# Performance work log

Measured on AMD Instinct MI355X. Metric: run time of the kernel, lower is better.

## Reference

```python
import jax, jax.numpy as jnp
import numpy as np

DIM = 1024
N_HEADS = 16
HEAD_DIM = DIM // N_HEADS
B, T = 2, 2048
ROPE_THETA = 32.0
EPS = 1e-6


def precompute_freqs_1d(dim, seq_len, theta):
    freqs = theta ** (-jnp.arange(0, dim, 2, dtype=jnp.float32) / dim)  # [dim/2]
    t = jnp.arange(seq_len, dtype=jnp.float32)
    ang = t[:, None] * freqs[None, :]  # [T, dim/2]
    return jnp.cos(ang), jnp.sin(ang)


def setup_inputs() -> dict:
    key = jax.random.key(0)
    k1, k2, k3, k4, k5 = jax.random.split(key, 5)
    x = jax.random.normal(k1, (B, T, DIM), dtype=jnp.float32)
    w_qkv = jax.random.normal(k2, (3 * DIM, DIM), dtype=jnp.float32) * (DIM ** -0.5)
    w_proj = jax.random.normal(k3, (DIM, DIM), dtype=jnp.float32) * (DIM ** -0.5)
    q_norm_w = 1.0 + 0.1 * jax.random.normal(k4, (HEAD_DIM,), dtype=jnp.float32)
    k_norm_w = 1.0 + 0.1 * jax.random.normal(k5, (HEAD_DIM,), dtype=jnp.float32)
    return {"x": x, "w_qkv": w_qkv, "w_proj": w_proj,
            "q_norm_w": q_norm_w, "k_norm_w": k_norm_w}


def _rms_norm(t, w):
    # t: [B,H,T,hd]; normalize over last dim
    var = jnp.mean(t * t, axis=-1, keepdims=True)
    return t * jax.lax.rsqrt(var + EPS) * w


def _rope(q, k, cos, sin):
    # cos/sin: [T, hd/2] -> [1,1,T,hd/2]
    cos = cos[None, None]
    sin = sin[None, None]
    q1, q2 = jnp.split(q, 2, axis=-1)
    k1, k2 = jnp.split(k, 2, axis=-1)
    q_out = jnp.concatenate([q1 * cos - q2 * sin, q2 * cos + q1 * sin], axis=-1)
    k_out = jnp.concatenate([k1 * cos - k2 * sin, k2 * cos + k1 * sin], axis=-1)
    return q_out, k_out


def reference(x, w_qkv, w_proj, q_norm_w, k_norm_w):
    Bc, Tc, C = x.shape
    scale = HEAD_DIM ** -0.5
    qkv = x @ w_qkv.T  # [B,T,3*C]
    qkv = qkv.reshape(Bc, Tc, 3, N_HEADS, HEAD_DIM).transpose(2, 0, 3, 1, 4)
    q, k, v = qkv[0], qkv[1], qkv[2]  # each [B,H,T,hd]
    q = _rms_norm(q, q_norm_w)
    k = _rms_norm(k, k_norm_w)
    cos, sin = precompute_freqs_1d(HEAD_DIM, Tc, ROPE_THETA)
    q, k = _rope(q, k, cos, sin)
    attn = jnp.einsum('bhqd,bhkd->bhqk', q, k) * scale
    causal = jnp.triu(jnp.ones((Tc, Tc), dtype=bool), k=1)
    attn = jnp.where(causal, -jnp.inf, attn)
    attn = jax.nn.softmax(attn, axis=-1)
    out = jnp.einsum('bhqk,bhkd->bhqd', attn, v)  # [B,H,T,hd]
    out = out.transpose(0, 2, 1, 3).reshape(Bc, Tc, C)
    return out @ w_proj.T
```

## Files before the change

### kernel.cpp

```cpp
#include <hip/hip_runtime.h>
#include <hip/hip_bf16.h>

#define DIM   1024
#define NH    16
#define HD    64
#define BB    2
#define TT    2048
#define BT    (BB*TT)
#define BHN   (BB*NH)

typedef __attribute__((ext_vector_type(8))) __bf16 bf16x8;
typedef __attribute__((ext_vector_type(4))) float  f32x4;

__device__ __forceinline__ unsigned short f2bf(float f) {
    unsigned int u = __float_as_uint(f);
    u = (u + 0x7fffu + ((u >> 16) & 1u)) >> 16;
    return (unsigned short)u;
}

__device__ __forceinline__ void gload_lds16(const unsigned short* g, unsigned short* l) {
    __builtin_amdgcn_global_load_lds(
        (const __attribute__((address_space(1))) unsigned int*)g,
        (__attribute__((address_space(3))) unsigned int*)l, 16, 0, 0);
}

__global__ __launch_bounds__(256) void cvt_bf16(const float* __restrict__ in,
                                                unsigned short* __restrict__ out, int n) {
    int i = blockIdx.x * 256 + threadIdx.x;
    int base = i * 8;
    if (base >= n) return;
    float4 a = *reinterpret_cast<const float4*>(in + base);
    float4 b = *reinterpret_cast<const float4*>(in + base + 4);
    uint4 o;
    o.x = (unsigned)f2bf(a.x) | ((unsigned)f2bf(a.y) << 16);
    o.y = (unsigned)f2bf(a.z) | ((unsigned)f2bf(a.w) << 16);
    o.z = (unsigned)f2bf(b.x) | ((unsigned)f2bf(b.y) << 16);
    o.w = (unsigned)f2bf(b.z) | ((unsigned)f2bf(b.w) << 16);
    *reinterpret_cast<uint4*>(out + base) = o;
}

__global__ __launch_bounds__(256) void build_rope(float* __restrict__ cosT,
                                                  float* __restrict__ sinT) {
    int i = blockIdx.x * 256 + threadIdx.x;
    if (i >= TT * 32) return;
    int t = i >> 5, j = i & 31;
    float freq = exp2f(-5.0f * (float)j * (1.0f / 32.0f));
    float ang  = (float)t * freq;
    cosT[i] = cosf(ang);
    sinT[i] = sinf(ang);
}

__global__ __launch_bounds__(256) void gemm_bt(const unsigned short* __restrict__ A,
                                               const unsigned short* __restrict__ Bt,
                                               float* __restrict__ C,
                                               int M, int N, int K) {
    __shared__ alignas(16) unsigned short sA[128 * 64];
    __shared__ alignas(16) unsigned short sB[128 * 64];
    const int t    = threadIdx.x;
    const int nb   = N >> 7;
    const int m0   = (blockIdx.x / nb) << 7;
    const int n0   = (blockIdx.x % nb) << 7;
    const int w    = t >> 6, lane = t & 63;
    const int wr   = w >> 1, wc = w & 1;
    const int lrow = lane & 15, lk = lane >> 4;
    const int r_   = t >> 3;
    const int c_   = t & 7;
    const int pg   = c_ ^ (r_ & 7);

    f32x4 acc[4][4] = {};

    for (int kt = 0; kt < K; kt += 64) {
        __syncthreads();
#pragma unroll
        for (int i = 0; i < 4; i++) {
            gload_lds16(A  + (size_t)(m0 + i * 32 + r_) * K + kt + pg * 8, sA + i * 2048 + w * 512);
            gload_lds16(Bt + (size_t)(n0 + i * 32 + r_) * K + kt + pg * 8, sB + i * 2048 + w * 512);
        }
        __syncthreads();
#pragma unroll
        for (int ks = 0; ks < 2; ks++) {
            bf16x8 af[4], bfr[4];
#pragma unroll
            for (int mi = 0; mi < 4; mi++) {
                int rowa = wr * 64 + mi * 16 + lrow;
                int ga   = (ks * 4 + lk) ^ (rowa & 7);
                af[mi]   = *reinterpret_cast<const bf16x8*>(&sA[rowa * 64 + ga * 8]);
                int rowb = wc * 64 + mi * 16 + lrow;
                int gb   = (ks * 4 + lk) ^ (rowb & 7);
                bfr[mi]  = *reinterpret_cast<const bf16x8*>(&sB[rowb * 64 + gb * 8]);
            }
#pragma unroll
            for (int mi = 0; mi < 4; mi++)
#pragma unroll
                for (int ni = 0; ni < 4; ni++)
                    acc[mi][ni] = __builtin_amdgcn_mfma_f32_16x16x32_bf16(af[mi], bfr[ni], acc[mi][ni], 0, 0, 0);
        }
    }
#pragma unroll
    for (int mi = 0; mi < 4; mi++)
#pragma unroll
        for (int ni = 0; ni < 4; ni++) {
            int row = m0 + wr * 64 + mi * 16 + lk * 4;
            int col = n0 + wc * 64 + ni * 16 + lrow;
#pragma unroll
            for (int i = 0; i < 4; i++)
                C[(size_t)(row + i) * N + col] = acc[mi][ni][i];
        }
}

__global__ __launch_bounds__(256) void norm_rope(const float* __restrict__ qkv,
                                                 const float* __restrict__ cosT,
                                                 const float* __restrict__ sinT,
                                                 const float* __restrict__ qw,
                                                 const float* __restrict__ kw,
                                                 unsigned short* __restrict__ Qo,
                                                 unsigned short* __restrict__ Ko,
                                                 unsigned short* __restrict__ Vo) {
    int wv = threadIdx.x >> 6, lane = threadIdx.x & 63;
    int rid = blockIdx.x * 4 + wv;
    int sel = rid >> 16;
    int rem = rid & 65535;
    int h   = rem & 15;
    int bt  = rem >> 4;
    int tp  = bt & (TT - 1);
    int b   = bt >> 11;
    float v = qkv[(size_t)bt * 3072 + sel * 1024 + h * 64 + lane];
    unsigned short* dst = (sel == 0) ? Qo : ((sel == 1) ? Ko : Vo);
    size_t didx = ((size_t)(b * NH + h) * TT + tp) * 64 + lane;
    float outv;
    if (sel < 2) {
        float ss = v * v;
#pragma unroll
        for (int m = 32; m; m >>= 1) ss += __shfl_xor(ss, m);
        float r = rsqrtf(ss * (1.0f / 64.0f) + 1e-6f);
        const float* wgt = sel ? kw : qw;
        float nv = v * r * wgt[lane];
        float other = __shfl_xor(nv, 32);
        int j = lane & 31;
        float c = cosT[tp * 32 + j], s = sinT[tp * 32 + j];
        outv = (lane < 32) ? (nv * c - other * s) : (nv * c + other * s);
        if (sel == 0) outv *= 0.125f * 1.4426950408889634f;
    } else {
        outv = v;
    }
    dst[didx] = f2bf(outv);
}

__global__ __launch_bounds__(256) void transpose_v(const unsigned short* __restrict__ Vb,
                                                   unsigned short* __restrict__ Vt) {
    __shared__ unsigned short s[64 * 68];
    const int t0 = blockIdx.x * 64, bh = blockIdx.y;
    const unsigned short* src = Vb + (size_t)bh * TT * 64;
    const int r = threadIdx.x >> 2, g4 = threadIdx.x & 3;
#pragma unroll
    for (int p = 0; p < 2; p++) {
        int g = g4 + p * 4;
        *reinterpret_cast<uint4*>(&s[r * 68 + g * 8]) =
            *reinterpret_cast<const uint4*>(src + (size_t)(t0 + r) * 64 + g * 8);
    }
    __syncthreads();
#pragma unroll
    for (int p = 0; p < 2; p++) {
        int tt = (g4 + p * 4) * 8;
        unsigned short tmp[8];
#pragma unroll
        for (int j = 0; j < 8; j++) tmp[j] = s[(tt + j) * 68 + r];
        *reinterpret_cast<uint4*>(Vt + ((size_t)bh * 64 + r) * TT + t0 + tt) =
            *reinterpret_cast<uint4*>(tmp);
    }
}

__global__ __launch_bounds__(256) void attn_fwd(const unsigned short* __restrict__ Qm,
                                                const unsigned short* __restrict__ Km,
                                                const unsigned short* __restrict__ Vt,
                                                unsigned short* __restrict__ Om) {
    __shared__ alignas(16) unsigned short sQ[64 * 68];
    __shared__ alignas(16) unsigned short sK[64 * 68];
    __shared__ alignas(16) unsigned short sVT[64 * 68];
    __shared__ alignas(16) unsigned short sP[4][16 * 68];
    const int bh = blockIdx.y;
    const int qt = (blockIdx.x + blockIdx.y) & 31;
    const int b = bh >> 4, h = bh & 15;
    const unsigned short* Qp = Qm + (size_t)bh * TT * 64;
    const unsigned short* Kp = Km + (size_t)bh * TT * 64;
    const unsigned short* Vp = Vt + (size_t)bh * 64 * TT;
    const int t = threadIdx.x, wv = t >> 6, lane = t & 63;
    const int lrow = lane & 15, lk = lane >> 4;
    const int r_ = t >> 3, c_ = t & 7;
    const int d_ = t >> 2, g_ = t & 3;

#pragma unroll
    for (int i = 0; i < 2; i++) {
        int r = i * 32 + r_;
        *reinterpret_cast<uint4*>(&sQ[r * 68 + c_ * 8]) =
            *reinterpret_cast<const uint4*>(Qp + (size_t)(qt * 64 + r) * 64 + c_ * 8);
    }
    uint4 kreg[2], vreg[2];
#pragma unroll
    for (int i = 0; i < 2; i++)
        kreg[i] = *reinterpret_cast<const uint4*>(Kp + (size_t)(i * 32 + r_) * 64 + c_ * 8);
#pragma unroll
    for (int p = 0; p < 2; p++)
        vreg[p] = *reinterpret_cast<const uint4*>(Vp + (size_t)d_ * TT + (g_ + p * 4) * 8);
#pragma unroll
    for (int i = 0; i < 2; i++)
        *reinterpret_cast<uint4*>(&sK[(i * 32 + r_) * 68 + c_ * 8]) = kreg[i];
#pragma unroll
    for (int p = 0; p < 2; p++)
        *reinterpret_cast<uint4*>(&sVT[d_ * 68 + (g_ + p * 4) * 8]) = vreg[p];
    __syncthreads();

    bf16x8 aq0 = *reinterpret_cast<const bf16x8*>(&sQ[(wv * 16 + lrow) * 68 + lk * 8]);
    bf16x8 aq1 = *reinterpret_cast<const bf16x8*>(&sQ[(wv * 16 + lrow) * 68 + 32 + lk * 8]);

    f32x4 o[4] = {};
    float mrun[4], lsum[4];
#pragma unroll
    for (int i = 0; i < 4; i++) { mrun[i] = -__builtin_inff(); lsum[i] = 0.0f; }

    for (int kt = 0; kt <= qt; kt++) {
        const bool more = (kt < qt);
        if (more) {
#pragma unroll
            for (int i = 0; i < 2; i++)
                kreg[i] = *reinterpret_cast<const uint4*>(Kp + (size_t)((kt + 1) * 64 + i * 32 + r_) * 64 + c_ * 8);
#pragma unroll
            for (int p = 0; p < 2; p++)
                vreg[p] = *reinterpret_cast<const uint4*>(Vp + (size_t)d_ * TT + (kt + 1) * 64 + (g_ + p * 4) * 8);
        }

        f32x4 s[4];
#pragma unroll
        for (int nt = 0; nt < 4; nt++) {
            f32x4 z = {0.f, 0.f, 0.f, 0.f};
            z = __builtin_amdgcn_mfma_f32_16x16x32_bf16(
                aq0, *reinterpret_cast<const bf16x8*>(&sK[(nt * 16 + lrow) * 68 + lk * 8]), z, 0, 0, 0);
            z = __builtin_amdgcn_mfma_f32_16x16x32_bf16(
                aq1, *reinterpret_cast<const bf16x8*>(&sK[(nt * 16 + lrow) * 68 + 32 + lk * 8]), z, 0, 0, 0);
            s[nt] = z;
        }
        if (kt == qt) {
#pragma unroll
            for (int nt = 0; nt < 4; nt++)
#pragma unroll
                for (int i = 0; i < 4; i++)
                    if (nt * 16 + lrow > wv * 16 + lk * 4 + i) s[nt][i] = -__builtin_inff();
        }

        float pm[4];
#pragma unroll
        for (int i = 0; i < 4; i++)
            pm[i] = fmaxf(fmaxf(s[0][i], s[1][i]), fmaxf(s[2][i], s[3][i]));
        bool skip = __all(pm[0] <= mrun[0] + 8.0f && pm[1] <= mrun[1] + 8.0f &&
                          pm[2] <= mrun[2] + 8.0f && pm[3] <= mrun[3] + 8.0f);
        if (!skip) {
#pragma unroll
            for (int i = 0; i < 4; i++) {
                float a = pm[i];
#pragma unroll
                for (int msk = 8; msk; msk >>= 1) a = fmaxf(a, __shfl_xor(a, msk));
                float mn = fmaxf(mrun[i], a);
                float fsc = exp2f(mrun[i] - mn);
                mrun[i] = mn;
                lsum[i] *= fsc;
#pragma unroll
                for (int dt = 0; dt < 4; dt++) o[dt][i] *= fsc;
            }
        }
#pragma unroll
        for (int nt = 0; nt < 4; nt++)
#pragma unroll
            for (int i = 0; i < 4; i++) {
                float p = exp2f(s[nt][i] - mrun[i]);
                s[nt][i] = p;
            }
#pragma unroll
        for (int i = 0; i < 4; i++)
            lsum[i] += (s[0][i] + s[1][i]) + (s[2][i] + s[3][i]);

        unsigned short* myP = &sP[wv][0];
#pragma unroll
        for (int nt = 0; nt < 4; nt++)
#pragma unroll
            for (int i = 0; i < 4; i++)
                myP[(lk * 4 + i) * 68 + nt * 16 + lrow] = f2bf(s[nt][i]);
        bf16x8 pa0 = *reinterpret_cast<const bf16x8*>(&myP[lrow * 68 + lk * 8]);
        bf16x8 pa1 = *reinterpret_cast<const bf16x8*>(&myP[lrow * 68 + 32 + lk * 8]);
#pragma unroll
        for (int dt = 0; dt < 4; dt++) {
            o[dt] = __builtin_amdgcn_mfma_f32_16x16x32_bf16(
                pa0, *reinterpret_cast<const bf16x8*>(&sVT[(dt * 16 + lrow) * 68 + lk * 8]), o[dt], 0, 0, 0);
            o[dt] = __builtin_amdgcn_mfma_f32_16x16x32_bf16(
                pa1, *reinterpret_cast<const bf16x8*>(&sVT[(dt * 16 + lrow) * 68 + 32 + lk * 8]), o[dt], 0, 0, 0);
        }

        __syncthreads();
        if (more) {
#pragma unroll
            for (int i = 0; i < 2; i++)
                *reinterpret_cast<uint4*>(&sK[(i * 32 + r_) * 68 + c_ * 8]) = kreg[i];
#pragma unroll
            for (int p = 0; p < 2; p++)
                *reinterpret_cast<uint4*>(&sVT[d_ * 68 + (g_ + p * 4) * 8]) = vreg[p];
            __syncthreads();
        }
    }

    float inv[4];
#pragma unroll
    for (int i = 0; i < 4; i++) {
        float a = lsum[i];
#pragma unroll
        for (int msk = 8; msk; msk >>= 1) a += __shfl_xor(a, msk);
        inv[i] = 1.0f / a;
    }
    int qrow = qt * 64 + wv * 16 + lk * 4;
#pragma unroll
    for (int dt = 0; dt < 4; dt++)
#pragma unroll
        for (int i = 0; i < 4; i++) {
            size_t idx = ((size_t)(b * TT + qrow + i)) * 1024 + h * 64 + dt * 16 + lrow;
            Om[idx] = f2bf(o[dt][i] * inv[i]);
        }
}

extern "C" void kernel_launch(void* const* d_in, const int* in_sizes, int n_in,
                              void* d_out, int out_size, void* d_ws, size_t ws_size,
                              hipStream_t stream) {
    const float* x      = (const float*)d_in[0];
    const float* w_qkv  = (const float*)d_in[1];
    const float* w_proj = (const float*)d_in[2];
    const float* qw     = (const float*)d_in[3];
    const float* kw     = (const float*)d_in[4];
    float* out = (float*)d_out;
    char* ws = (char*)d_ws;

    unsigned short* xb     = (unsigned short*)(ws + 0);
    unsigned short* wqkvb  = (unsigned short*)(ws + 8388608);
    unsigned short* wprojb = (unsigned short*)(ws + 14680064);
    float*          qkvf   = (float*)(ws + 16777216);
    unsigned short* Vtb    = (unsigned short*)(ws + 16777216);
    unsigned short* Qb     = (unsigned short*)(ws + 67108864);
    unsigned short* Kb     = (unsigned short*)(ws + 75497472);
    unsigned short* Vb     = (unsigned short*)(ws + 83886080);
    float*          cosT   = (float*)(ws + 92274688);
    float*          sinT   = (float*)(ws + 92536832);
    unsigned short* attnb  = xb;

    cvt_bf16<<<2048, 256, 0, stream>>>(x, xb, BT * DIM);
    cvt_bf16<<<1536, 256, 0, stream>>>(w_qkv, wqkvb, 3 * DIM * DIM);
    cvt_bf16<<<512, 256, 0, stream>>>(w_proj, wprojb, DIM * DIM);
    build_rope<<<256, 256, 0, stream>>>(cosT, sinT);
    gemm_bt<<<(BT / 128) * (3 * DIM / 128), 256, 0, stream>>>(xb, wqkvb, qkvf, BT, 3 * DIM, DIM);
    norm_rope<<<3 * BT * NH / 4, 256, 0, stream>>>(qkvf, cosT, sinT, qw, kw, Qb, Kb, Vb);
    transpose_v<<<dim3(TT / 64, BHN), 256, 0, stream>>>(Vb, Vtb);
    attn_fwd<<<dim3(TT / 64, BHN), 256, 0, stream>>>(Qb, Kb, Vtb, attnb);
    gemm_bt<<<(BT / 128) * (DIM / 128), 256, 0, stream>>>(attnb, wprojb, out, BT, DIM, DIM);
    (void)in_sizes; (void)n_in; (void)out_size; (void)ws_size;
}
```

Before: 304.3 us.

## Load K/V tiles directly to LDS with XOR-swizzled layout in attention

```diff
diff --git a/kernel.cpp b/kernel.cpp
--- a/kernel.cpp
+++ b/kernel.cpp
@@ -175,8 +175,8 @@
                                                 const unsigned short* __restrict__ Vt,
                                                 unsigned short* __restrict__ Om) {
     __shared__ alignas(16) unsigned short sQ[64 * 68];
-    __shared__ alignas(16) unsigned short sK[64 * 68];
-    __shared__ alignas(16) unsigned short sVT[64 * 68];
+    __shared__ alignas(16) unsigned short sK[64 * 64];
+    __shared__ alignas(16) unsigned short sVT[64 * 64];
     __shared__ alignas(16) unsigned short sP[4][16 * 68];
     const int bh = blockIdx.y;
     const int qt = (blockIdx.x + blockIdx.y) & 31;
@@ -186,8 +186,9 @@
     const unsigned short* Vp = Vt + (size_t)bh * 64 * TT;
     const int t = threadIdx.x, wv = t >> 6, lane = t & 63;
     const int lrow = lane & 15, lk = lane >> 4;
-    const int r_ = t >> 3, c_ = t & 7;
-    const int d_ = t >> 2, g_ = t & 3;
+    const int r_ = t >> 3;
+    const int c_ = t & 7;
+    const int pg = c_ ^ (r_ & 7);
 
 #pragma unroll
     for (int i = 0; i < 2; i++) {
@@ -195,21 +196,7 @@
         *reinterpret_cast<uint4*>(&sQ[r * 68 + c_ * 8]) =
             *reinterpret_cast<const uint4*>(Qp + (size_t)(qt * 64 + r) * 64 + c_ * 8);
     }
-    uint4 kreg[2], vreg[2];
-#pragma unroll
-    for (int i = 0; i < 2; i++)
-        kreg[i] = *reinterpret_cast<const uint4*>(Kp + (size_t)(i * 32 + r_) * 64 + c_ * 8);
-#pragma unroll
-    for (int p = 0; p < 2; p++)
-        vreg[p] = *reinterpret_cast<const uint4*>(Vp + (size_t)d_ * TT + (g_ + p * 4) * 8);
-#pragma unroll
-    for (int i = 0; i < 2; i++)
-        *reinterpret_cast<uint4*>(&sK[(i * 32 + r_) * 68 + c_ * 8]) = kreg[i];
-#pragma unroll
-    for (int p = 0; p < 2; p++)
-        *reinterpret_cast<uint4*>(&sVT[d_ * 68 + (g_ + p * 4) * 8]) = vreg[p];
     __syncthreads();
-
     bf16x8 aq0 = *reinterpret_cast<const bf16x8*>(&sQ[(wv * 16 + lrow) * 68 + lk * 8]);
     bf16x8 aq1 = *reinterpret_cast<const bf16x8*>(&sQ[(wv * 16 + lrow) * 68 + 32 + lk * 8]);
 
@@ -219,24 +206,23 @@
     for (int i = 0; i < 4; i++) { mrun[i] = -__builtin_inff(); lsum[i] = 0.0f; }
 
     for (int kt = 0; kt <= qt; kt++) {
-        const bool more = (kt < qt);
-        if (more) {
-#pragma unroll
-            for (int i = 0; i < 2; i++)
-                kreg[i] = *reinterpret_cast<const uint4*>(Kp + (size_t)((kt + 1) * 64 + i * 32 + r_) * 64 + c_ * 8);
-#pragma unroll
-            for (int p = 0; p < 2; p++)
-                vreg[p] = *reinterpret_cast<const uint4*>(Vp + (size_t)d_ * TT + (kt + 1) * 64 + (g_ + p * 4) * 8);
-        }
+        __syncthreads();
+#pragma unroll
+        for (int i = 0; i < 2; i++) {
+            gload_lds16(Kp + (size_t)(kt * 64 + i * 32 + r_) * 64 + pg * 8, sK + i * 2048 + wv * 512);
+            gload_lds16(Vp + (size_t)(i * 32 + r_) * TT + kt * 64 + pg * 8, sVT + i * 2048 + wv * 512);
+        }
+        __syncthreads();
 
         f32x4 s[4];
 #pragma unroll
         for (int nt = 0; nt < 4; nt++) {
+            int row = nt * 16 + lrow;
             f32x4 z = {0.f, 0.f, 0.f, 0.f};
             z = __builtin_amdgcn_mfma_f32_16x16x32_bf16(
-                aq0, *reinterpret_cast<const bf16x8*>(&sK[(nt * 16 + lrow) * 68 + lk * 8]), z, 0, 0, 0);
+                aq0, *reinterpret_cast<const bf16x8*>(&sK[row * 64 + (lk ^ (row & 7)) * 8]), z, 0, 0, 0);
             z = __builtin_amdgcn_mfma_f32_16x16x32_bf16(
-                aq1, *reinterpret_cast<const bf16x8*>(&sK[(nt * 16 + lrow) * 68 + 32 + lk * 8]), z, 0, 0, 0);
+                aq1, *reinterpret_cast<const bf16x8*>(&sK[row * 64 + ((4 + lk) ^ (row & 7)) * 8]), z, 0, 0, 0);
             s[nt] = z;
         }
         if (kt == qt) {
@@ -270,10 +256,8 @@
 #pragma unroll
         for (int nt = 0; nt < 4; nt++)
 #pragma unroll
-            for (int i = 0; i < 4; i++) {
-                float p = exp2f(s[nt][i] - mrun[i]);
-                s[nt][i] = p;
-            }
+            for (int i = 0; i < 4; i++)
+                s[nt][i] = exp2f(s[nt][i] - mrun[i]);
 #pragma unroll
         for (int i = 0; i < 4; i++)
             lsum[i] += (s[0][i] + s[1][i]) + (s[2][i] + s[3][i]);
@@ -288,21 +272,11 @@
         bf16x8 pa1 = *reinterpret_cast<const bf16x8*>(&myP[lrow * 68 + 32 + lk * 8]);
 #pragma unroll
         for (int dt = 0; dt < 4; dt++) {
+            int row = dt * 16 + lrow;
             o[dt] = __builtin_amdgcn_mfma_f32_16x16x32_bf16(
-                pa0, *reinterpret_cast<const bf16x8*>(&sVT[(dt * 16 + lrow) * 68 + lk * 8]), o[dt], 0, 0, 0);
+                pa0, *reinterpret_cast<const bf16x8*>(&sVT[row * 64 + (lk ^ (row & 7)) * 8]), o[dt], 0, 0, 0);
             o[dt] = __builtin_amdgcn_mfma_f32_16x16x32_bf16(
-                pa1, *reinterpret_cast<const bf16x8*>(&sVT[(dt * 16 + lrow) * 68 + 32 + lk * 8]), o[dt], 0, 0, 0);
-        }
-
-        __syncthreads();
-        if (more) {
-#pragma unroll
-            for (int i = 0; i < 2; i++)
-                *reinterpret_cast<uint4*>(&sK[(i * 32 + r_) * 68 + c_ * 8]) = kreg[i];
-#pragma unroll
-            for (int p = 0; p < 2; p++)
-                *reinterpret_cast<uint4*>(&sVT[d_ * 68 + (g_ + p * 4) * 8]) = vreg[p];
-            __syncthreads();
+                pa1, *reinterpret_cast<const bf16x8*>(&sVT[row * 64 + ((4 + lk) ^ (row & 7)) * 8]), o[dt], 0, 0, 0);
         }
     }
 
```

New measurement: 256.1 us. -15.8%, faster.
